# Kernel optimization log

Hardware: AMD Instinct MI355X
Metric: run time of the kernel (lower is better)

The kernel has to match this reference:

```python
import jax, jax.numpy as jnp
import numpy as np

N = 2048
IMG = 128
FOCAL = float(IMG)


def quat_to_rot(q):
    # q = (w, x, y, z), normalized -> (N, 3, 3) rotation matrices
    q = q / jnp.linalg.norm(q, axis=-1, keepdims=True)
    w, x, y, z = q[..., 0], q[..., 1], q[..., 2], q[..., 3]
    R = jnp.stack([
        1 - 2 * (y * y + z * z), 2 * (x * y - w * z), 2 * (x * z + w * y),
        2 * (x * y + w * z), 1 - 2 * (x * x + z * z), 2 * (y * z - w * x),
        2 * (x * z - w * y), 2 * (y * z + w * x), 1 - 2 * (x * x + y * y),
    ], axis=-1).reshape(q.shape[:-1] + (3, 3))
    return R


def setup_inputs() -> dict:
    key = jax.random.key(0)
    ks = jax.random.split(key, 4)
    return {
        'means': jax.random.normal(ks[0], (N, 3), jnp.float32) * 0.5,
        'log_scales': jnp.full((N, 3), -2.0, jnp.float32) + 0.1 * jax.random.normal(ks[1], (N, 3), jnp.float32),
        'rotations': jax.random.normal(ks[2], (N, 4), jnp.float32) + jnp.array([2.0, 0.0, 0.0, 0.0], jnp.float32),
        'opacity_logit': jnp.zeros((N, 1), jnp.float32),
        'color_pre': jax.random.normal(ks[3], (N, 3), jnp.float32) * 0.5,
        'cam_pos': jnp.array([0.0, 0.0, 5.0], jnp.float32),
        'look_at': jnp.zeros((3,), jnp.float32),
    }


def reference(means, log_scales, rotations, opacity_logit, color_pre, cam_pos, look_at):
    # --- activations of learned params ---
    scales = jnp.exp(log_scales)                      # (N, 3)
    opac = jax.nn.sigmoid(opacity_logit)[:, 0]        # (N,)
    colors = jax.nn.sigmoid(color_pre)                # (N, 3)

    # --- 3D covariance: Sigma = R S S^T R^T ---
    R = quat_to_rot(rotations)                        # (N, 3, 3)
    M = R * scales[:, None, :]                        # R @ diag(s)
    cov3d = M @ jnp.swapaxes(M, -1, -2)               # (N, 3, 3)

    # --- camera basis (world -> camera) ---
    fwd = look_at - cam_pos
    fwd = fwd / jnp.linalg.norm(fwd)
    right = jnp.cross(fwd, jnp.array([0.0, 1.0, 0.0], jnp.float32))
    right = right / jnp.linalg.norm(right)
    up = jnp.cross(right, fwd)
    Wm = jnp.stack([right, up, -fwd], axis=0)         # (3, 3)

    # --- project means ---
    means_cam = (means - cam_pos[None]) @ Wm.T        # (N, 3)
    depths = -means_cam[:, 2]
    x_cam = means_cam[:, 0] / (-means_cam[:, 2] + 1e-8)
    y_cam = means_cam[:, 1] / (-means_cam[:, 2] + 1e-8)
    means_2d = jnp.stack([x_cam * FOCAL + IMG / 2, -y_cam * FOCAL + IMG / 2], axis=-1)

    # --- EWA 2D covariance ---
    cov_cam = jnp.einsum('ab,nbc,dc->nad', Wm, cov3d, Wm)      # W Sigma W^T
    z_sq = jnp.maximum(depths ** 2, 0.01)[:, None, None]
    cov_2d = cov_cam[:, :2, :2] * FOCAL ** 2 / z_sq + 0.3 * jnp.eye(2, dtype=jnp.float32)

    # --- depth sort (front to back) ---
    idx = jnp.argsort(depths)
    d_s = depths[idx]
    m2d = means_2d[idx]
    c2d = cov_2d[idx]
    col_s = colors[idx]
    op_s = opac[idx]

    # culling -> mask instead of dynamic filtering (jit-friendly, same math)
    valid = ((d_s > 0.1)
             & (m2d[:, 0] > -IMG) & (m2d[:, 0] < 2 * IMG)
             & (m2d[:, 1] > -IMG) & (m2d[:, 1] < 2 * IMG)).astype(jnp.float32)

    a = c2d[:, 0, 0]
    b = c2d[:, 0, 1]
    d = c2d[:, 1, 1]
    det = jnp.maximum(a * d - b * b, 1e-6)
    cov_inv = jnp.stack([d, -b, -b, a], axis=-1).reshape(-1, 2, 2) / det[:, None, None]

    yy, xx = jnp.meshgrid(jnp.arange(IMG, dtype=jnp.float32),
                          jnp.arange(IMG, dtype=jnp.float32), indexing='ij')
    pixels = jnp.stack([xx, yy], axis=-1)             # (H, W, 2)

    def body(carry, g):
        image, T = carry
        mu, inv, col, op, v = g
        diff = pixels - mu                            # (H, W, 2)
        mahal = jnp.einsum('hwi,ij,hwj->hw', diff, inv, diff)
        alpha = jnp.minimum(op * jnp.exp(-0.5 * mahal), 0.99) * v
        image = image + (T * alpha)[..., None] * (col[None, None] - image)
        T = T * (1.0 - alpha)
        return (image, T), None

    init = (jnp.ones((IMG, IMG, 3), jnp.float32), jnp.ones((IMG, IMG), jnp.float32))
    (image, _), _ = jax.lax.scan(body, init, (m2d, cov_inv, col_s, op_s, valid))
    return jnp.clip(image, 0.0, 1.0)
```

## Files before the change

kernel.cpp:

```cpp
#include <hip/hip_runtime.h>
#include <hip/hip_bf16.h>
#include <hip/hip_fp16.h>

#define N_G   2048
#define IMGF  128.0f
#define RECF  8


typedef __fp16 half2_v __attribute__((ext_vector_type(2)));
union H2U { half2_v h2; float f; unsigned int u; };

static __device__ __forceinline__ unsigned int f32_bf16(float f) {
    unsigned int u = __float_as_uint(f);
    return (u + 0x7FFFu + ((u >> 16) & 1u)) >> 16;
}

__global__ void gs_preprocess(const float* __restrict__ means,
                              const float* __restrict__ log_scales,
                              const float* __restrict__ rotations,
                              const float* __restrict__ opacity_logit,
                              const float* __restrict__ color_pre,
                              const float* __restrict__ cam_pos,
                              const float* __restrict__ look_at,
                              float* __restrict__ rec,
                              unsigned long long* __restrict__ keys)
{
    int i = blockIdx.x * blockDim.x + threadIdx.x;
    if (i >= N_G) return;

    float cx = cam_pos[0], cy = cam_pos[1], cz = cam_pos[2];
    float fx = look_at[0] - cx, fy = look_at[1] - cy, fz = look_at[2] - cz;
    float fn = 1.0f / sqrtf(fx*fx + fy*fy + fz*fz);
    fx *= fn; fy *= fn; fz *= fn;
    float rx = -fz, ry = 0.0f, rz = fx;
    float rn = 1.0f / sqrtf(rx*rx + ry*ry + rz*rz);
    rx *= rn; ry *= rn; rz *= rn;
    float ux = ry*fz - rz*fy, uy = rz*fx - rx*fz, uz = rx*fy - ry*fx;

    float mx = means[3*i+0] - cx, my = means[3*i+1] - cy, mz = means[3*i+2] - cz;
    float m0 =  rx*mx + ry*my + rz*mz;
    float m1 =  ux*mx + uy*my + uz*mz;
    float m2 = -(fx*mx + fy*my + fz*mz);
    float d  = -m2;
    float invz = 1.0f / (-m2 + 1e-8f);
    float m2dx =  (m0 * invz) * IMGF + IMGF * 0.5f;
    float m2dy = -(m1 * invz) * IMGF + IMGF * 0.5f;

    float s0 = expf(log_scales[3*i+0]);
    float s1 = expf(log_scales[3*i+1]);
    float s2 = expf(log_scales[3*i+2]);
    float qw = rotations[4*i+0], qx = rotations[4*i+1],
          qy = rotations[4*i+2], qz = rotations[4*i+3];
    float qn = 1.0f / sqrtf(qw*qw + qx*qx + qy*qy + qz*qz);
    qw *= qn; qx *= qn; qy *= qn; qz *= qn;
    float R00 = 1-2*(qy*qy+qz*qz), R01 = 2*(qx*qy-qw*qz), R02 = 2*(qx*qz+qw*qy);
    float R10 = 2*(qx*qy+qw*qz), R11 = 1-2*(qx*qx+qz*qz), R12 = 2*(qy*qz-qw*qx);
    float R20 = 2*(qx*qz-qw*qy), R21 = 2*(qy*qz+qw*qx), R22 = 1-2*(qx*qx+qy*qy);
    float t0 = s0*s0, t1 = s1*s1, t2 = s2*s2;
    float C00 = R00*R00*t0 + R01*R01*t1 + R02*R02*t2;
    float C01 = R00*R10*t0 + R01*R11*t1 + R02*R12*t2;
    float C02 = R00*R20*t0 + R01*R21*t1 + R02*R22*t2;
    float C11 = R10*R10*t0 + R11*R11*t1 + R12*R12*t2;
    float C12 = R10*R20*t0 + R11*R21*t1 + R12*R22*t2;
    float C22 = R20*R20*t0 + R21*R21*t1 + R22*R22*t2;

    float v0 = C00*rx + C01*ry + C02*rz;
    float v1 = C01*rx + C11*ry + C12*rz;
    float v2 = C02*rx + C12*ry + C22*rz;
    float ca = rx*v0 + ry*v1 + rz*v2;
    float cb = ux*v0 + uy*v1 + uz*v2;
    float w0 = C00*ux + C01*uy + C02*uz;
    float w1 = C01*ux + C11*uy + C12*uz;
    float w2 = C02*ux + C12*uy + C22*uz;
    float cd = ux*w0 + uy*w1 + uz*w2;

    float z2 = fmaxf(d*d, 0.01f);
    float sc = (IMGF * IMGF) / z2;
    float a  = ca*sc + 0.3f;
    float b  = cb*sc;
    float dd = cd*sc + 0.3f;
    float det  = fmaxf(a*dd - b*b, 1e-6f);
    float idet = 1.0f / det;

    bool valid = (d > 0.1f) && (m2dx > -IMGF) && (m2dx < 2.0f*IMGF)
                            && (m2dy > -IMGF) && (m2dy < 2.0f*IMGF);

    float op = 1.0f / (1.0f + expf(-opacity_logit[i]));
    const float L2E = 1.4426950408889634f;
    float A2 = -0.5f * L2E * dd * idet;
    float B2 =          L2E * b  * idet;
    float D2 = -0.5f * L2E * a  * idet;
    float L  = valid ? log2f(op) : -1e10f;

    float cr = 1.0f / (1.0f + expf(-color_pre[3*i+0]));
    float cg = 1.0f / (1.0f + expf(-color_pre[3*i+1]));
    float cl = 1.0f / (1.0f + expf(-color_pre[3*i+2]));

    unsigned int w6 = f32_bf16(cr) | (f32_bf16(cg) << 16);
    unsigned int w7 = f32_bf16(cl);

    float4* r4 = (float4*)(rec + RECF*i);
    r4[0] = make_float4(m2dx, m2dy, A2, B2);
    r4[1] = make_float4(D2, L, __uint_as_float(w6), __uint_as_float(w7));

    unsigned int ub   = __float_as_uint(d);
    unsigned int mask = ((unsigned int)((int)ub >> 31)) | 0x80000000u;
    keys[i] = ((unsigned long long)(ub ^ mask) << 32) | (unsigned int)i;
}

__global__ void __launch_bounds__(256)
gs_rank_scatter(const unsigned long long* __restrict__ keys,
                const float* __restrict__ rec,
                float* __restrict__ srec)
{
    __shared__ __align__(16) unsigned long long sk[N_G];
    int t = threadIdx.x;

    const ulonglong2* k2 = (const ulonglong2*)keys;
    ulonglong2* s2 = (ulonglong2*)sk;
    #pragma unroll
    for (int q = 0; q < 4; ++q) s2[t + q*256] = k2[t + q*256];
    __syncthreads();

    int g   = (blockIdx.x << 5) | (t >> 3);
    int seg = t & 7;
    unsigned long long ki = sk[g];
    const ulonglong2* sseg = (const ulonglong2*)(sk + (seg << 8));
    int rank = 0;
    #pragma unroll 8
    for (int j = 0; j < 128; ++j) {
        ulonglong2 a = sseg[(j + seg * 17) & 127];
        rank += (int)(a.x < ki) + (int)(a.y < ki);
    }
    rank += __shfl_xor(rank, 1);
    rank += __shfl_xor(rank, 2);
    rank += __shfl_xor(rank, 4);

    int slot = ((rank & 31) << 6) | (rank >> 5);
    srec[slot * RECF + seg] = rec[g * RECF + seg];
}

__global__ void __launch_bounds__(256, 4)
gs_raster(const float* __restrict__ srec, float* __restrict__ out)
{
    int tid  = threadIdx.x;
    int lane = tid & 63;
    int wave = (blockIdx.x << 2) | (tid >> 6);
    int p0   = wave * 2;
    float px0 = (float)(p0 & 127);
    float px1 = px0 + 1.0f;
    float py  = (float)(p0 >> 7);

    float vp[32];
    float P0 = 1.0f, P1 = 1.0f;

    #pragma unroll
    for (int i = 0; i < 32; ++i) {
        const float* r = srec + (size_t)((i << 6) | lane) * RECF;
        float4 ra = *(const float4*)r;
        float2 rb = *(const float2*)(r + 4);
        float dy   = py - ra.y;
        float b2dy = ra.w * dy;
        float t2   = fmaf(rb.x * dy, dy, rb.y);
        float dx0  = px0 - ra.x;
        float dx1  = px1 - ra.x;
        float q0 = fmaf(dx0, fmaf(ra.z, dx0, b2dy), t2);
        float q1 = fmaf(dx1, fmaf(ra.z, dx1, b2dy), t2);
        float a0 = fminf(__builtin_amdgcn_exp2f(q0), 0.99f);
        float a1 = fminf(__builtin_amdgcn_exp2f(q1), 0.99f);
        float u0 = P0 * a0;  P0 *= (1.0f - a0);
        float u1 = P1 * a1;  P1 *= (1.0f - a1);
        H2U hp; hp.h2 = __builtin_amdgcn_cvt_pkrtz(u0, u1);
        vp[i] = hp.f;
    }

    float sp0 = P0, sp1 = P1;
    #pragma unroll
    for (int d = 1; d < 64; d <<= 1) {
        float y0 = __shfl_up(sp0, d);
        float y1 = __shfl_up(sp1, d);
        if (lane >= d) { sp0 *= y0; sp1 *= y1; }
    }
    float e0 = __shfl_up(sp0, 1);
    float e1 = __shfl_up(sp1, 1);
    float Tin0 = (lane == 0) ? 1.0f : e0;
    float Tin1 = (lane == 0) ? 1.0f : e1;

    float B0 = 1.0f, B1 = 1.0f;
    #pragma unroll
    for (int i = 0; i < 32; ++i) {
        H2U h; h.f = vp[i];
        B0 *= fmaf(-Tin0, (float)h.h2.x, 1.0f);
        B1 *= fmaf(-Tin1, (float)h.h2.y, 1.0f);
    }

    float ss0 = B0, ss1 = B1;
    #pragma unroll
    for (int d = 1; d < 64; d <<= 1) {
        float y0 = __shfl_down(ss0, d);
        float y1 = __shfl_down(ss1, d);
        if (lane + d < 64) { ss0 *= y0; ss1 *= y1; }
    }
    float f0 = __shfl_down(ss0, 1);
    float f1 = __shfl_down(ss1, 1);
    float S0 = (lane == 63) ? 1.0f : f0;
    float S1 = (lane == 63) ? 1.0f : f1;

    float ar0 = 0.0f, ag0 = 0.0f, ab0 = 0.0f;
    float ar1 = 0.0f, ag1 = 0.0f, ab1 = 0.0f;
    #pragma unroll
    for (int i = 31; i >= 0; --i) {
        const float* r = srec + (size_t)((i << 6) | lane) * RECF;
        float2 cp = *(const float2*)(r + 6);
        unsigned int w6 = __float_as_uint(cp.x);
        unsigned int w7 = __float_as_uint(cp.y);
        float cr = __uint_as_float(w6 << 16);
        float cg = __uint_as_float(w6 & 0xFFFF0000u);
        float cb = __uint_as_float(w7 << 16);
        H2U h; h.f = vp[i];
        float u0  = Tin0 * (float)h.h2.x;
        float us0 = u0 * S0;
        ar0 = fmaf(us0, cr, ar0); ag0 = fmaf(us0, cg, ag0); ab0 = fmaf(us0, cb, ab0);
        S0 = fmaf(-u0, S0, S0);
        float u1  = Tin1 * (float)h.h2.y;
        float us1 = u1 * S1;
        ar1 = fmaf(us1, cr, ar1); ag1 = fmaf(us1, cg, ag1); ab1 = fmaf(us1, cb, ab1);
        S1 = fmaf(-u1, S1, S1);
    }

    #pragma unroll
    for (int d = 1; d < 64; d <<= 1) {
        ar0 += __shfl_xor(ar0, d); ag0 += __shfl_xor(ag0, d); ab0 += __shfl_xor(ab0, d);
        ar1 += __shfl_xor(ar1, d); ag1 += __shfl_xor(ag1, d); ab1 += __shfl_xor(ab1, d);
    }

    if (lane == 0) {
        float* o0 = out + (size_t)p0 * 3;
        o0[0] = fminf(fmaxf(S0 + ar0, 0.0f), 1.0f);
        o0[1] = fminf(fmaxf(S0 + ag0, 0.0f), 1.0f);
        o0[2] = fminf(fmaxf(S0 + ab0, 0.0f), 1.0f);
        o0[3] = fminf(fmaxf(S1 + ar1, 0.0f), 1.0f);
        o0[4] = fminf(fmaxf(S1 + ag1, 0.0f), 1.0f);
        o0[5] = fminf(fmaxf(S1 + ab1, 0.0f), 1.0f);
    }
}

extern "C" void kernel_launch(void* const* d_in, const int* in_sizes, int n_in,
                              void* d_out, int out_size, void* d_ws, size_t ws_size,
                              hipStream_t stream)
{
    const float* means         = (const float*)d_in[0];
    const float* log_scales    = (const float*)d_in[1];
    const float* rotations     = (const float*)d_in[2];
    const float* opacity_logit = (const float*)d_in[3];
    const float* color_pre     = (const float*)d_in[4];
    const float* cam_pos       = (const float*)d_in[5];
    const float* look_at       = (const float*)d_in[6];
    float* out = (float*)d_out;

    char* ws = (char*)d_ws;
    float*              rec  = (float*)(ws);
    unsigned long long* keys = (unsigned long long*)(ws + 65536);
    float*              srec = (float*)(ws + 65536 + 16384);

    hipLaunchKernelGGL(gs_preprocess, dim3(N_G / 256), dim3(256), 0, stream,
                       means, log_scales, rotations, opacity_logit, color_pre,
                       cam_pos, look_at, rec, keys);
    hipLaunchKernelGGL(gs_rank_scatter, dim3(N_G / 32), dim3(256), 0, stream,
                       keys, rec, srec);
    hipLaunchKernelGGL(gs_raster, dim3(2048), dim3(256), 0, stream,
                       srec, out);
}
```

Before: 115.9 us.

## Stage sorted Gaussian records in swizzled LDS before rasterization

Each raster block now copies the full 64 KB sorted record array into shared memory with an XOR swizzle, then reads the geometry and color fields from LDS instead of global/L2. This is meant to cut repeated global load latency across the two passes over the records. In exchange each block pays a 64 KB bulk copy plus a barrier, and the large LDS footprint limits how many blocks fit per CU. The occupancy hint of 4 blocks in launch bounds is dropped to match.

```diff
diff --git a/kernel.cpp b/kernel.cpp
--- a/kernel.cpp
+++ b/kernel.cpp
@@ -140,25 +140,41 @@
     srec[slot * RECF + seg] = rec[g * RECF + seg];
 }
 
-__global__ void __launch_bounds__(256, 4)
+__global__ void __launch_bounds__(256)
 gs_raster(const float* __restrict__ srec, float* __restrict__ out)
 {
+    __shared__ __align__(16) unsigned char sbuf[65536];
     int tid  = threadIdx.x;
     int lane = tid & 63;
+
+    {
+        const float4* g = (const float4*)srec;
+        #pragma unroll
+        for (int q = tid; q < 4096; q += 256) {
+            unsigned int byte = (unsigned int)q << 4;
+            unsigned int swz  = byte ^ (((byte >> 5) & 7u) << 4);
+            *(float4*)(sbuf + swz) = g[q];
+        }
+    }
+    __syncthreads();
+
     int wave = (blockIdx.x << 2) | (tid >> 6);
     int p0   = wave * 2;
     float px0 = (float)(p0 & 127);
     float px1 = px0 + 1.0f;
     float py  = (float)(p0 >> 7);
 
+    unsigned int xorv  = ((unsigned int)(lane & 7)) << 4;
+    unsigned int lbase = (((unsigned int)lane) << 5) ^ xorv;
+
     float vp[32];
     float P0 = 1.0f, P1 = 1.0f;
 
     #pragma unroll
     for (int i = 0; i < 32; ++i) {
-        const float* r = srec + (size_t)((i << 6) | lane) * RECF;
-        float4 ra = *(const float4*)r;
-        float2 rb = *(const float2*)(r + 4);
+        unsigned int a0 = (unsigned int)(i << 11) + lbase;
+        float4 ra = *(const float4*)(sbuf + a0);
+        float2 rb = *(const float2*)(sbuf + (a0 ^ 16u));
         float dy   = py - ra.y;
         float b2dy = ra.w * dy;
         float t2   = fmaf(rb.x * dy, dy, rb.y);
@@ -166,10 +182,10 @@
         float dx1  = px1 - ra.x;
         float q0 = fmaf(dx0, fmaf(ra.z, dx0, b2dy), t2);
         float q1 = fmaf(dx1, fmaf(ra.z, dx1, b2dy), t2);
-        float a0 = fminf(__builtin_amdgcn_exp2f(q0), 0.99f);
-        float a1 = fminf(__builtin_amdgcn_exp2f(q1), 0.99f);
-        float u0 = P0 * a0;  P0 *= (1.0f - a0);
-        float u1 = P1 * a1;  P1 *= (1.0f - a1);
+        float a0f = fminf(__builtin_amdgcn_exp2f(q0), 0.99f);
+        float a1f = fminf(__builtin_amdgcn_exp2f(q1), 0.99f);
+        float u0 = P0 * a0f;  P0 *= (1.0f - a0f);
+        float u1 = P1 * a1f;  P1 *= (1.0f - a1f);
         H2U hp; hp.h2 = __builtin_amdgcn_cvt_pkrtz(u0, u1);
         vp[i] = hp.f;
     }
@@ -210,8 +226,8 @@
     float ar1 = 0.0f, ag1 = 0.0f, ab1 = 0.0f;
     #pragma unroll
     for (int i = 31; i >= 0; --i) {
-        const float* r = srec + (size_t)((i << 6) | lane) * RECF;
-        float2 cp = *(const float2*)(r + 6);
+        unsigned int a0 = (unsigned int)(i << 11) + lbase;
+        float2 cp = *(const float2*)(sbuf + (a0 ^ 16u) + 8u);
         unsigned int w6 = __float_as_uint(cp.x);
         unsigned int w7 = __float_as_uint(cp.y);
         float cr = __uint_as_float(w6 << 16);
```

After: 107.1 us. -7.6%, faster.
